# Optimization experiments

Measured on AMD Instinct MI355X. Metric: run time of the kernel, lower is better.

The kernel has to match this reference:

```python
import jax, jax.numpy as jnp
import numpy as np

B = 65536          # batch
E = 512            # embedding_dim
SL = 128           # speed_latent_dim
H = 256            # hidden_size
NB = 6             # num_branch
D = E + SL         # 640, branch input dim


def _linear_init(k, din, dout):
    bound = 1.0 / np.sqrt(din)
    kw, kb = jax.random.split(k)
    W = jax.random.uniform(kw, (din, dout), minval=-bound, maxval=bound, dtype=jnp.float32)
    b = jax.random.uniform(kb, (dout,), minval=-bound, maxval=bound, dtype=jnp.float32)
    return W, b


def setup_inputs() -> dict:
    key = jax.random.key(0)
    ks = jax.random.split(key, 10)
    embedding = jax.random.normal(ks[0], (B, E), dtype=jnp.float32)
    speed = jax.random.uniform(ks[1], (B, 1), dtype=jnp.float32)
    command = jax.random.randint(ks[2], (B,), 1, NB + 1)  # values in 1..6

    # speed_in: Linear(1,H) -> ReLU -> Linear(H,SL)
    si_W1, si_b1 = _linear_init(ks[3], 1, H)
    si_W2, si_b2 = _linear_init(ks[4], H, SL)

    # speed_out: Linear(D,H) -> ReLU -> Linear(H,H) -> ReLU -> Linear(H,1)
    so_W1, so_b1 = _linear_init(ks[5], D, H)
    so_W2, so_b2 = _linear_init(ks[6], H, H)
    so_W3, so_b3 = _linear_init(ks[7], H, 1)

    # NB branches, each Linear(D,H)->ReLU->Linear(H,H)->ReLU->Linear(H,3)->Sigmoid
    def mk_branch(k):
        k1, k2, k3 = jax.random.split(k, 3)
        W1, b1 = _linear_init(k1, D, H)
        W2, b2 = _linear_init(k2, H, H)
        W3, b3 = _linear_init(k3, H, 3)
        return W1, b1, W2, b2, W3, b3

    bW1, bb1, bW2, bb2, bW3, bb3 = jax.vmap(mk_branch)(jax.random.split(ks[8], NB))

    return {
        "embedding": embedding, "speed": speed, "command": command,
        "si_W1": si_W1, "si_b1": si_b1, "si_W2": si_W2, "si_b2": si_b2,
        "bW1": bW1, "bb1": bb1, "bW2": bW2, "bb2": bb2, "bW3": bW3, "bb3": bb3,
        "so_W1": so_W1, "so_b1": so_b1, "so_W2": so_W2, "so_b2": so_b2,
        "so_W3": so_W3, "so_b3": so_b3,
    }


def reference(embedding, speed, command,
              si_W1, si_b1, si_W2, si_b2,
              bW1, bb1, bW2, bb2, bW3, bb3,
              so_W1, so_b1, so_W2, so_b2, so_W3, so_b3):
    # speed_in MLP and concat
    s = jax.nn.relu(speed @ si_W1 + si_b1) @ si_W2 + si_b2          # [B, SL]
    emb = jnp.concatenate([embedding, s], axis=1)                    # [B, D]

    # all branches computed densely (as in the torch module), then one-hot mask
    h1 = jax.nn.relu(jnp.einsum('bd,ndh->nbh', emb, bW1) + bb1[:, None, :])   # [NB,B,H]
    h2 = jax.nn.relu(jnp.einsum('nbh,nhk->nbk', h1, bW2) + bb2[:, None, :])   # [NB,B,H]
    out = jax.nn.sigmoid(jnp.einsum('nbk,nko->nbo', h2, bW3) + bb3[:, None, :])  # [NB,B,3]

    mask = (jnp.arange(NB)[:, None] == (command - 1)[None, :]).astype(out.dtype)  # [NB,B]
    control_pred = jnp.sum(out * mask[:, :, None], axis=0)           # [B, 3]

    # speed prediction head
    sp = jax.nn.relu(emb @ so_W1 + so_b1)
    sp = jax.nn.relu(sp @ so_W2 + so_b2)
    speed_pred = sp @ so_W3 + so_b3                                  # [B, 1]

    return control_pred, speed_pred
```

## Files before the change

### kernel.cpp

```cpp
#include <hip/hip_runtime.h>
#include <cstdint>
#include <cstddef>

typedef _Float16 f16;
typedef f16 f16x8 __attribute__((ext_vector_type(8)));
typedef float f32x4 __attribute__((ext_vector_type(4)));

#define B_ROWS 65536
#define NT_BRANCH 1030
#define NT_SPEED 1024

constexpr size_t OFF_SF16   = 0;
constexpr size_t SZ_SF16    = (size_t)B_ROWS * 128 * 2;
constexpr size_t OFF_SIW2T  = OFF_SF16 + SZ_SF16;
constexpr size_t SZ_SIW2T   = (size_t)128 * 256 * 2;
constexpr size_t OFF_BW1T   = OFF_SIW2T + SZ_SIW2T;
constexpr size_t SZ_BW1T    = (size_t)6 * 256 * 640 * 2;
constexpr size_t OFF_BW2T   = OFF_BW1T + SZ_BW1T;
constexpr size_t SZ_BW2T    = (size_t)6 * 256 * 256 * 2;
constexpr size_t OFF_SOW1T  = OFF_BW2T + SZ_BW2T;
constexpr size_t SZ_SOW1T   = (size_t)256 * 640 * 2;
constexpr size_t OFF_SOW2T  = OFF_SOW1T + SZ_SOW1T;
constexpr size_t SZ_SOW2T   = (size_t)256 * 256 * 2;
constexpr size_t OFF_BW3T16 = OFF_SOW2T + SZ_SOW2T;
constexpr size_t SZ_BW3T16  = (size_t)6 * 16 * 256 * 2;
constexpr size_t OFF_SOW3T16= OFF_BW3T16 + SZ_BW3T16;
constexpr size_t SZ_SOW3T16 = (size_t)16 * 256 * 2;
constexpr size_t OFF_COUNTS = OFF_SOW3T16 + SZ_SOW3T16;
constexpr size_t OFF_CURSORS= OFF_COUNTS + 256;
constexpr size_t OFF_BINBASE= OFF_CURSORS + 256;
constexpr size_t OFF_TILECMD= OFF_BINBASE + 256;
constexpr size_t OFF_PERM   = OFF_TILECMD + 4352;
constexpr size_t WS_NEEDED  = OFF_PERM + (size_t)NT_BRANCH * 64 * 4;

#define MFMA16(a, b, c) __builtin_amdgcn_mfma_f32_16x16x32_f16(a, b, c, 0, 0, 0)
#define BARSYNC() asm volatile("s_waitcnt lgkmcnt(0)\n\ts_barrier" ::: "memory")

__global__ void prep_kernel(const float* __restrict__ siW2,
                            const float* __restrict__ bW1,
                            const float* __restrict__ bW2,
                            const float* __restrict__ soW1,
                            const float* __restrict__ soW2,
                            const float* __restrict__ bW3,
                            const float* __restrict__ soW3,
                            f16* __restrict__ siW2T, f16* __restrict__ bW1T,
                            f16* __restrict__ bW2T, f16* __restrict__ soW1T,
                            f16* __restrict__ soW2T,
                            f16* __restrict__ bW3T16, f16* __restrict__ soW3T16,
                            int* __restrict__ counts, int* __restrict__ cursors,
                            int* __restrict__ perm)
{
    const int bx = blockIdx.x;
    const int tx = threadIdx.x, ty = threadIdx.y;
    const int tid = ty * 32 + tx;
    if (bx >= 1601) {
        const int ib = bx - 1601;
        const int idx = ib * 256 + tid;
        if (idx < NT_BRANCH * 64) perm[idx] = -1;
        if (ib == 0 && tid < 6) { counts[tid] = 0; cursors[tid] = 0; }
        return;
    }
    if (bx == 1600) {
        for (int i = tid; i < 6 * 16 * 256; i += 256) {
            const int c = i >> 12, rem = i & 4095, n = rem >> 8, k = rem & 255;
            bW3T16[i] = (n < 3) ? (f16)bW3[((size_t)c * 256 + k) * 3 + n] : (f16)0;
        }
        for (int i = tid; i < 16 * 256; i += 256) {
            const int n = i >> 8, k = i & 255;
            soW3T16[i] = (n == 0) ? (f16)soW3[k] : (f16)0;
        }
        return;
    }
    const float* in; f16* out; int R, C, lb;
    if (bx < 960)       { int m = bx / 160;        lb = bx - m * 160;       in = bW1 + (size_t)m * 640 * 256; out = bW1T + (size_t)m * 640 * 256; R = 640; C = 256; }
    else if (bx < 1344) { int m = (bx - 960) / 64; lb = (bx - 960) - m * 64; in = bW2 + (size_t)m * 256 * 256; out = bW2T + (size_t)m * 256 * 256; R = 256; C = 256; }
    else if (bx < 1504) { lb = bx - 1344; in = soW1; out = soW1T; R = 640; C = 256; }
    else if (bx < 1568) { lb = bx - 1504; in = soW2; out = soW2T; R = 256; C = 256; }
    else                { lb = bx - 1568; in = siW2; out = siW2T; R = 256; C = 128; }
    const int txt = C >> 5;
    const int c0 = (lb % txt) << 5;
    const int r0 = (lb / txt) << 5;
    __shared__ float tile[32][33];
    #pragma unroll
    for (int i = 0; i < 4; ++i)
        tile[tx][ty + 8 * i] = in[(size_t)(r0 + ty + 8 * i) * C + c0 + tx];
    __syncthreads();
    #pragma unroll
    for (int i = 0; i < 4; ++i)
        out[(size_t)(c0 + ty + 8 * i) * R + r0 + tx] = (f16)tile[ty + 8 * i][tx];
}

__global__ __launch_bounds__(256) void speedin_kernel(
    const float* __restrict__ speed,
    const float* __restrict__ siW1, const float* __restrict__ sib1,
    const f16* __restrict__ siW2T, const float* __restrict__ sib2,
    const int* __restrict__ cmd,
    f16* __restrict__ sF16, int* __restrict__ counts)
{
    __shared__ f16 H[64 * 264];
    __shared__ float spd[64];
    __shared__ int h[6];
    const int tid = threadIdx.x;
    const int rb = blockIdx.x * 64;
    if (tid < 6) h[tid] = 0;
    __syncthreads();
    if (tid < 64) {
        spd[tid] = speed[rb + tid];
        atomicAdd(&h[cmd[rb + tid] - 1], 1);
    }
    __syncthreads();
    if (tid < 6 && h[tid] > 0) atomicAdd(&counts[tid], h[tid]);
    {
        const float w1 = siW1[tid], b1v = sib1[tid];
        #pragma unroll 4
        for (int r = 0; r < 64; ++r) {
            float hv = spd[r] * w1 + b1v;
            H[r * 264 + tid] = (f16)(hv > 0.f ? hv : 0.f);
        }
    }
    __syncthreads();
    const int w = tid >> 6, lane = tid & 63, lq = lane >> 4, l16 = lane & 15;
    const int nb = w * 32;
    f32x4 acc[4][2];
    #pragma unroll
    for (int mt = 0; mt < 4; ++mt)
        #pragma unroll
        for (int nt = 0; nt < 2; ++nt)
            acc[mt][nt] = (f32x4){0.f, 0.f, 0.f, 0.f};
    for (int ks = 0; ks < 8; ++ks) {
        const int koff = ks * 32 + lq * 8;
        f16x8 af[4], bf[2];
        #pragma unroll
        for (int mt = 0; mt < 4; ++mt)
            af[mt] = *(const f16x8*)(&H[(mt * 16 + l16) * 264 + koff]);
        #pragma unroll
        for (int nt = 0; nt < 2; ++nt)
            bf[nt] = *(const f16x8*)(siW2T + (size_t)(nb + nt * 16 + l16) * 256 + koff);
        #pragma unroll
        for (int mt = 0; mt < 4; ++mt)
            #pragma unroll
            for (int nt = 0; nt < 2; ++nt)
                acc[mt][nt] = MFMA16(af[mt], bf[nt], acc[mt][nt]);
    }
    #pragma unroll
    for (int mt = 0; mt < 4; ++mt)
        #pragma unroll
        for (int nt = 0; nt < 2; ++nt) {
            const int n = nb + nt * 16 + l16;
            const float bv = sib2[n];
            #pragma unroll
            for (int r2 = 0; r2 < 4; ++r2) {
                const int m = mt * 16 + lq * 4 + r2;
                sF16[(size_t)(rb + m) * 128 + n] = (f16)(acc[mt][nt][r2] + bv);
            }
        }
}

__global__ void plan_kernel(const int* __restrict__ counts,
                            int* __restrict__ binBase, int* __restrict__ tile_cmd) {
    __shared__ int tbase[7];
    if (threadIdx.x == 0) {
        int base = 0, tb = 0;
        for (int c = 0; c < 6; ++c) {
            binBase[c] = base;
            tbase[c] = tb;
            const int nt = (counts[c] + 63) >> 6;
            tb += nt;
            base += nt << 6;
        }
        tbase[6] = tb;
    }
    __syncthreads();
    for (int t = threadIdx.x; t < NT_BRANCH; t += 256) {
        int c = -1;
        #pragma unroll
        for (int j = 0; j < 6; ++j)
            if (t >= tbase[j] && t < tbase[j + 1]) c = j;
        tile_cmd[t] = c;
    }
}

__global__ void place_kernel(const int* __restrict__ cmd,
                             const int* __restrict__ binBase,
                             int* __restrict__ cursors, int* __restrict__ perm) {
    __shared__ int lcnt[6], lbase[6];
    const int tid = threadIdx.x;
    if (tid < 6) lcnt[tid] = 0;
    __syncthreads();
    const int i = blockIdx.x * 256 + tid;
    const int c = cmd[i] - 1;
    const int myr = atomicAdd(&lcnt[c], 1);
    __syncthreads();
    if (tid < 6) lbase[tid] = atomicAdd(&cursors[tid], lcnt[tid]);
    __syncthreads();
    perm[binBase[c] + lbase[c] + myr] = i;
}

__device__ __forceinline__ f16x8 stage_load(const float* __restrict__ srcF,
                                            const f16* __restrict__ srcH,
                                            int kc, int p) {
    if (kc < 8) {
        const float* s = srcF + kc * 64 + p * 8;
        const float4 f0 = ((const float4*)s)[0];
        const float4 f1 = ((const float4*)s)[1];
        f16x8 v;
        v[0] = (f16)f0.x; v[1] = (f16)f0.y; v[2] = (f16)f0.z; v[3] = (f16)f0.w;
        v[4] = (f16)f1.x; v[5] = (f16)f1.y; v[6] = (f16)f1.z; v[7] = (f16)f1.w;
        return v;
    } else {
        return *(const f16x8*)(srcH + (kc - 8) * 64 + p * 8);
    }
}

__global__ __launch_bounds__(512, 4) void heads_kernel(
    const float* __restrict__ emb,
    const f16* __restrict__ sF16,
    const int* __restrict__ perm, const int* __restrict__ tile_cmd,
    const f16* __restrict__ bW1T, const f16* __restrict__ bW2T,
    const f16* __restrict__ bW3T16,
    const float* __restrict__ bb1, const float* __restrict__ bb2,
    const float* __restrict__ bb3,
    const f16* __restrict__ soW1T, const f16* __restrict__ soW2T,
    const f16* __restrict__ soW3T16,
    const float* __restrict__ sob1, const float* __restrict__ sob2,
    const float* __restrict__ sob3,
    float* __restrict__ out)
{
    __shared__ f16 smem[16896];
    __shared__ int rowIdx[64];
    const int bx = blockIdx.x;
    const int tid = threadIdx.x;
    const bool is_speed = (bx >= NT_BRANCH);
    const f16 *W1T, *W2T, *W3T;
    const float *bias1, *bias2, *bias3;
    if (is_speed) {
        const int t = bx - NT_BRANCH;
        if (tid < 64) rowIdx[tid] = t * 64 + tid;
        W1T = soW1T; W2T = soW2T; W3T = soW3T16;
        bias1 = sob1; bias2 = sob2; bias3 = sob3;
    } else {
        const int c = tile_cmd[bx];
        if (c < 0) return;
        if (tid < 64) rowIdx[tid] = perm[bx * 64 + tid];
        W1T = bW1T + (size_t)c * 256 * 640;
        W2T = bW2T + (size_t)c * 256 * 256;
        W3T = bW3T16 + (size_t)c * 16 * 256;
        bias1 = bb1 + c * 256; bias2 = bb2 + c * 256; bias3 = bb3 + c * 3;
    }
    __syncthreads();

    const int r = tid >> 3, p = tid & 7;
    int growS = rowIdx[r]; if (growS < 0) growS = 0;
    const float* srcF = emb + (size_t)growS * 512;
    const f16*   srcH = sF16 + (size_t)growS * 128;
    const int pOff = r * 72 + p * 8;

    const int w = tid >> 6, lane = tid & 63, lq = lane >> 4, l16 = lane & 15;
    const int nb = w * 32;
    const f16* brow[2];
    #pragma unroll
    for (int nt = 0; nt < 2; ++nt)
        brow[nt] = W1T + (size_t)(nb + nt * 16 + l16) * 640;

    f32x4 acc[4][2];
    #pragma unroll
    for (int mt = 0; mt < 4; ++mt)
        #pragma unroll
        for (int nt = 0; nt < 2; ++nt)
            acc[mt][nt] = (f32x4){0.f, 0.f, 0.f, 0.f};

    f16x8 sreg[4];
    f16x8 Bb[2][2][2];
    #pragma unroll
    for (int j = 0; j < 4; ++j)
        sreg[j] = stage_load(srcF, srcH, j, p);
    #pragma unroll
    for (int ks = 0; ks < 2; ++ks)
        #pragma unroll
        for (int nt = 0; nt < 2; ++nt) {
            Bb[0][ks][nt] = *(const f16x8*)(brow[nt] + 0 * 64 + ks * 32 + lq * 8);
            Bb[1][ks][nt] = *(const f16x8*)(brow[nt] + 1 * 64 + ks * 32 + lq * 8);
        }
    *(f16x8*)(smem + pOff) = sreg[0];
    BARSYNC();
    #pragma unroll
    for (int kc = 0; kc < 10; ++kc) {
        f16* cur = smem + (kc & 1) * 4608;
        if (kc < 9)
            *(f16x8*)(smem + ((kc + 1) & 1) * 4608 + pOff) = sreg[(kc + 1) & 3];
        if (kc < 6)
            sreg[kc & 3] = stage_load(srcF, srcH, kc + 4, p);
        #pragma unroll
        for (int ks = 0; ks < 2; ++ks) {
            f16x8 a[4];
            #pragma unroll
            for (int mt = 0; mt < 4; ++mt)
                a[mt] = *(const f16x8*)(cur + (mt * 16 + l16) * 72 + ks * 32 + lq * 8);
            #pragma unroll
            for (int mt = 0; mt < 4; ++mt)
                #pragma unroll
                for (int nt = 0; nt < 2; ++nt)
                    acc[mt][nt] = MFMA16(a[mt], Bb[kc & 1][ks][nt], acc[mt][nt]);
        }
        if (kc < 8) {
            #pragma unroll
            for (int ks = 0; ks < 2; ++ks)
                #pragma unroll
                for (int nt = 0; nt < 2; ++nt)
                    Bb[kc & 1][ks][nt] = *(const f16x8*)(brow[nt] + (kc + 2) * 64 + ks * 32 + lq * 8);
        }
        BARSYNC();
    }

    const f16* brow2[2];
    #pragma unroll
    for (int nt = 0; nt < 2; ++nt)
        brow2[nt] = W2T + (size_t)(nb + nt * 16 + l16) * 256;
    f16x8 Bd[2][2];
    #pragma unroll
    for (int nt = 0; nt < 2; ++nt)
        Bd[0][nt] = *(const f16x8*)(brow2[nt] + lq * 8);

    #pragma unroll
    for (int mt = 0; mt < 4; ++mt)
        #pragma unroll
        for (int nt = 0; nt < 2; ++nt) {
            const int n = nb + nt * 16 + l16;
            const float bv = bias1[n];
            #pragma unroll
            for (int r2 = 0; r2 < 4; ++r2) {
                const int m = mt * 16 + lq * 4 + r2;
                const float v = acc[mt][nt][r2] + bv;
                smem[m * 264 + n] = (f16)(v > 0.f ? v : 0.f);
            }
            acc[mt][nt] = (f32x4){0.f, 0.f, 0.f, 0.f};
        }
    BARSYNC();

    #pragma unroll
    for (int ks = 0; ks < 8; ++ks) {
        if (ks < 7) {
            #pragma unroll
            for (int nt = 0; nt < 2; ++nt)
                Bd[(ks + 1) & 1][nt] = *(const f16x8*)(brow2[nt] + (ks + 1) * 32 + lq * 8);
        }
        f16x8 a[4];
        #pragma unroll
        for (int mt = 0; mt < 4; ++mt)
            a[mt] = *(const f16x8*)(&smem[(mt * 16 + l16) * 264 + ks * 32 + lq * 8]);
        #pragma unroll
        for (int mt = 0; mt < 4; ++mt)
            #pragma unroll
            for (int nt = 0; nt < 2; ++nt)
                acc[mt][nt] = MFMA16(a[mt], Bd[ks & 1][nt], acc[mt][nt]);
    }
    BARSYNC();
    #pragma unroll
    for (int mt = 0; mt < 4; ++mt)
        #pragma unroll
        for (int nt = 0; nt < 2; ++nt) {
            const int n = nb + nt * 16 + l16;
            const float bv = bias2[n];
            #pragma unroll
            for (int r2 = 0; r2 < 4; ++r2) {
                const int m = mt * 16 + lq * 4 + r2;
                const float v = acc[mt][nt][r2] + bv;
                smem[m * 264 + n] = (f16)(v > 0.f ? v : 0.f);
            }
        }
    BARSYNC();
    if (w < 4) {
        f32x4 acc3 = (f32x4){0.f, 0.f, 0.f, 0.f};
        const f16* w3row = W3T + (size_t)l16 * 256;
        #pragma unroll
        for (int ks = 0; ks < 8; ++ks) {
            const int koff = ks * 32 + lq * 8;
            const f16x8 af = *(const f16x8*)(&smem[(w * 16 + l16) * 264 + koff]);
            const f16x8 bf = *(const f16x8*)(w3row + koff);
            acc3 = MFMA16(af, bf, acc3);
        }
        const int orow = w * 16 + lq * 4;
        if (!is_speed) {
            if (l16 < 3) {
                const float b3 = bias3[l16];
                #pragma unroll
                for (int r2 = 0; r2 < 4; ++r2) {
                    const int g = rowIdx[orow + r2];
                    if (g >= 0)
                        out[(size_t)g * 3 + l16] = 1.f / (1.f + __expf(-(acc3[r2] + b3)));
                }
            }
        } else {
            if (l16 == 0) {
                const float b3 = bias3[0];
                #pragma unroll
                for (int r2 = 0; r2 < 4; ++r2)
                    out[(size_t)3 * B_ROWS + rowIdx[orow + r2]] = acc3[r2] + b3;
            }
        }
    }
}

extern "C" void kernel_launch(void* const* d_in, const int* in_sizes, int n_in,
                              void* d_out, int out_size, void* d_ws, size_t ws_size,
                              hipStream_t stream) {
    (void)in_sizes; (void)n_in; (void)out_size; (void)ws_size;
    const float* embedding = (const float*)d_in[0];
    const float* speed     = (const float*)d_in[1];
    const int*   command   = (const int*)d_in[2];
    const float* si_W1 = (const float*)d_in[3];
    const float* si_b1 = (const float*)d_in[4];
    const float* si_W2 = (const float*)d_in[5];
    const float* si_b2 = (const float*)d_in[6];
    const float* bW1   = (const float*)d_in[7];
    const float* bb1   = (const float*)d_in[8];
    const float* bW2   = (const float*)d_in[9];
    const float* bb2   = (const float*)d_in[10];
    const float* bW3   = (const float*)d_in[11];
    const float* bb3   = (const float*)d_in[12];
    const float* so_W1 = (const float*)d_in[13];
    const float* so_b1 = (const float*)d_in[14];
    const float* so_W2 = (const float*)d_in[15];
    const float* so_b2 = (const float*)d_in[16];
    const float* so_W3 = (const float*)d_in[17];
    const float* so_b3 = (const float*)d_in[18];
    float* out = (float*)d_out;

    char* ws = (char*)d_ws;
    f16* sF16   = (f16*)(ws + OFF_SF16);
    f16* siW2T  = (f16*)(ws + OFF_SIW2T);
    f16* bW1T   = (f16*)(ws + OFF_BW1T);
    f16* bW2T   = (f16*)(ws + OFF_BW2T);
    f16* soW1T  = (f16*)(ws + OFF_SOW1T);
    f16* soW2T  = (f16*)(ws + OFF_SOW2T);
    f16* bW3T16 = (f16*)(ws + OFF_BW3T16);
    f16* soW3T16= (f16*)(ws + OFF_SOW3T16);
    int* counts = (int*)(ws + OFF_COUNTS);
    int* cursors= (int*)(ws + OFF_CURSORS);
    int* binBase= (int*)(ws + OFF_BINBASE);
    int* tile_cmd = (int*)(ws + OFF_TILECMD);
    int* perm   = (int*)(ws + OFF_PERM);

    prep_kernel<<<1859, dim3(32, 8), 0, stream>>>(
        si_W2, bW1, bW2, so_W1, so_W2, bW3, so_W3,
        siW2T, bW1T, bW2T, soW1T, soW2T, bW3T16, soW3T16,
        counts, cursors, perm);
    speedin_kernel<<<1024, 256, 0, stream>>>(
        speed, si_W1, si_b1, siW2T, si_b2, command, sF16, counts);
    plan_kernel<<<1, 256, 0, stream>>>(counts, binBase, tile_cmd);
    place_kernel<<<256, 256, 0, stream>>>(command, binBase, cursors, perm);
    heads_kernel<<<NT_BRANCH + NT_SPEED, 512, 0, stream>>>(
        embedding, sF16, perm, tile_cmd,
        bW1T, bW2T, bW3T16, bb1, bb2, bb3,
        soW1T, soW2T, soW3T16, so_b1, so_b2, so_b3, out);
}
```

Before: 380.9 us.

## Stage layer-1 activations in two half-K LDS chunks instead of double-buffered 64-col tiles

Replaces the per-64-column double-buffered LDS pipeline for the first GEMM with two large staging phases. Each phase loads 320 columns of the activation row, converts them to fp16 and stores them in a 64x328 LDS tile. The second half is prefetched into registers while the first half is being consumed. This cuts the block-wide barriers from about ten to a handful and issues the global loads in larger batches. In exchange it uses more LDS and more registers per thread (float4 staging arrays), which may lower occupancy under launch_bounds(512,4).

```diff
diff --git a/kernel.cpp b/kernel.cpp
--- a/kernel.cpp
+++ b/kernel.cpp
@@ -196,19 +196,40 @@
     perm[binBase[c] + lbase[c] + myr] = i;
 }
 
-__device__ __forceinline__ f16x8 stage_load(const float* __restrict__ srcF,
-                                            const f16* __restrict__ srcH,
-                                            int kc, int p) {
-    if (kc < 8) {
-        const float* s = srcF + kc * 64 + p * 8;
-        const float4 f0 = ((const float4*)s)[0];
-        const float4 f1 = ((const float4*)s)[1];
-        f16x8 v;
-        v[0] = (f16)f0.x; v[1] = (f16)f0.y; v[2] = (f16)f0.z; v[3] = (f16)f0.w;
-        v[4] = (f16)f1.x; v[5] = (f16)f1.y; v[6] = (f16)f1.z; v[7] = (f16)f1.w;
-        return v;
-    } else {
-        return *(const f16x8*)(srcH + (kc - 8) * 64 + p * 8);
+template<bool PREF>
+__device__ __forceinline__ void kc_iter(const f16* __restrict__ smem,
+                                        const f16* __restrict__ brow0,
+                                        const f16* __restrict__ brow1,
+                                        f16x8 (&Bb)[2][2], f32x4 (&acc)[4][2],
+                                        int LCOL, int NGCOL, int l16, int lq)
+{
+    f16x8 Bn[2][2];
+    if (PREF) {
+        #pragma unroll
+        for (int ks = 0; ks < 2; ++ks) {
+            Bn[ks][0] = *(const f16x8*)(brow0 + NGCOL + ks * 32 + lq * 8);
+            Bn[ks][1] = *(const f16x8*)(brow1 + NGCOL + ks * 32 + lq * 8);
+        }
+    }
+    f16x8 a_[2][4];
+    #pragma unroll
+    for (int ks = 0; ks < 2; ++ks)
+        #pragma unroll
+        for (int mt = 0; mt < 4; ++mt)
+            a_[ks][mt] = *(const f16x8*)(smem + (mt * 16 + l16) * 328 + LCOL + ks * 32 + lq * 8);
+    #pragma unroll
+    for (int ks = 0; ks < 2; ++ks)
+        #pragma unroll
+        for (int mt = 0; mt < 4; ++mt)
+            #pragma unroll
+            for (int nt = 0; nt < 2; ++nt)
+                acc[mt][nt] = MFMA16(a_[ks][mt], Bb[ks][nt], acc[mt][nt]);
+    if (PREF) {
+        #pragma unroll
+        for (int ks = 0; ks < 2; ++ks)
+            #pragma unroll
+            for (int nt = 0; nt < 2; ++nt)
+                Bb[ks][nt] = Bn[ks][nt];
     }
 }
 
@@ -226,7 +247,7 @@
     const float* __restrict__ sob3,
     float* __restrict__ out)
 {
-    __shared__ f16 smem[16896];
+    __shared__ f16 smem[64 * 328];
     __shared__ int rowIdx[64];
     const int bx = blockIdx.x;
     const int tid = threadIdx.x;
@@ -253,14 +274,36 @@
     int growS = rowIdx[r]; if (growS < 0) growS = 0;
     const float* srcF = emb + (size_t)growS * 512;
     const f16*   srcH = sF16 + (size_t)growS * 128;
-    const int pOff = r * 72 + p * 8;
+    const int wOff = r * 328 + p * 8;
 
     const int w = tid >> 6, lane = tid & 63, lq = lane >> 4, l16 = lane & 15;
     const int nb = w * 32;
-    const f16* brow[2];
-    #pragma unroll
-    for (int nt = 0; nt < 2; ++nt)
-        brow[nt] = W1T + (size_t)(nb + nt * 16 + l16) * 640;
+    const f16* brow0 = W1T + (size_t)(nb + l16) * 640;
+    const f16* brow1 = W1T + (size_t)(nb + 16 + l16) * 640;
+
+    f16x8 Bb[2][2];
+    #pragma unroll
+    for (int ks = 0; ks < 2; ++ks) {
+        Bb[ks][0] = *(const f16x8*)(brow0 + ks * 32 + lq * 8);
+        Bb[ks][1] = *(const f16x8*)(brow1 + ks * 32 + lq * 8);
+    }
+
+    float4 s0[5][2];
+    #pragma unroll
+    for (int c = 0; c < 5; ++c) {
+        const float* s = srcF + c * 64 + p * 8;
+        s0[c][0] = ((const float4*)s)[0];
+        s0[c][1] = ((const float4*)s)[1];
+    }
+    #pragma unroll
+    for (int c = 0; c < 5; ++c) {
+        f16x8 v;
+        v[0] = (f16)s0[c][0].x; v[1] = (f16)s0[c][0].y;
+        v[2] = (f16)s0[c][0].z; v[3] = (f16)s0[c][0].w;
+        v[4] = (f16)s0[c][1].x; v[5] = (f16)s0[c][1].y;
+        v[6] = (f16)s0[c][1].z; v[7] = (f16)s0[c][1].w;
+        *(f16x8*)(smem + wOff + c * 64) = v;
+    }
 
     f32x4 acc[4][2];
     #pragma unroll
@@ -269,48 +312,45 @@
         for (int nt = 0; nt < 2; ++nt)
             acc[mt][nt] = (f32x4){0.f, 0.f, 0.f, 0.f};
 
-    f16x8 sreg[4];
-    f16x8 Bb[2][2][2];
-    #pragma unroll
-    for (int j = 0; j < 4; ++j)
-        sreg[j] = stage_load(srcF, srcH, j, p);
-    #pragma unroll
-    for (int ks = 0; ks < 2; ++ks)
-        #pragma unroll
-        for (int nt = 0; nt < 2; ++nt) {
-            Bb[0][ks][nt] = *(const f16x8*)(brow[nt] + 0 * 64 + ks * 32 + lq * 8);
-            Bb[1][ks][nt] = *(const f16x8*)(brow[nt] + 1 * 64 + ks * 32 + lq * 8);
-        }
-    *(f16x8*)(smem + pOff) = sreg[0];
-    BARSYNC();
-    #pragma unroll
-    for (int kc = 0; kc < 10; ++kc) {
-        f16* cur = smem + (kc & 1) * 4608;
-        if (kc < 9)
-            *(f16x8*)(smem + ((kc + 1) & 1) * 4608 + pOff) = sreg[(kc + 1) & 3];
-        if (kc < 6)
-            sreg[kc & 3] = stage_load(srcF, srcH, kc + 4, p);
-        #pragma unroll
-        for (int ks = 0; ks < 2; ++ks) {
-            f16x8 a[4];
-            #pragma unroll
-            for (int mt = 0; mt < 4; ++mt)
-                a[mt] = *(const f16x8*)(cur + (mt * 16 + l16) * 72 + ks * 32 + lq * 8);
-            #pragma unroll
-            for (int mt = 0; mt < 4; ++mt)
-                #pragma unroll
-                for (int nt = 0; nt < 2; ++nt)
-                    acc[mt][nt] = MFMA16(a[mt], Bb[kc & 1][ks][nt], acc[mt][nt]);
-        }
-        if (kc < 8) {
-            #pragma unroll
-            for (int ks = 0; ks < 2; ++ks)
-                #pragma unroll
-                for (int nt = 0; nt < 2; ++nt)
-                    Bb[kc & 1][ks][nt] = *(const f16x8*)(brow[nt] + (kc + 2) * 64 + ks * 32 + lq * 8);
-        }
-        BARSYNC();
-    }
+    BARSYNC();
+
+    kc_iter<true>(smem, brow0, brow1, Bb, acc,   0,  64, l16, lq);
+    kc_iter<true>(smem, brow0, brow1, Bb, acc,  64, 128, l16, lq);
+    kc_iter<true>(smem, brow0, brow1, Bb, acc, 128, 192, l16, lq);
+
+    float4 s1[3][2];
+    f16x8 t1[2];
+    #pragma unroll
+    for (int c = 0; c < 3; ++c) {
+        const float* s = srcF + 320 + c * 64 + p * 8;
+        s1[c][0] = ((const float4*)s)[0];
+        s1[c][1] = ((const float4*)s)[1];
+    }
+    t1[0] = *(const f16x8*)(srcH + p * 8);
+    t1[1] = *(const f16x8*)(srcH + 64 + p * 8);
+
+    kc_iter<true>(smem, brow0, brow1, Bb, acc, 192, 256, l16, lq);
+    kc_iter<true>(smem, brow0, brow1, Bb, acc, 256, 320, l16, lq);
+
+    BARSYNC();
+    #pragma unroll
+    for (int c = 0; c < 3; ++c) {
+        f16x8 v;
+        v[0] = (f16)s1[c][0].x; v[1] = (f16)s1[c][0].y;
+        v[2] = (f16)s1[c][0].z; v[3] = (f16)s1[c][0].w;
+        v[4] = (f16)s1[c][1].x; v[5] = (f16)s1[c][1].y;
+        v[6] = (f16)s1[c][1].z; v[7] = (f16)s1[c][1].w;
+        *(f16x8*)(smem + wOff + c * 64) = v;
+    }
+    *(f16x8*)(smem + wOff + 192) = t1[0];
+    *(f16x8*)(smem + wOff + 256) = t1[1];
+    BARSYNC();
+
+    kc_iter<true >(smem, brow0, brow1, Bb, acc,   0, 384, l16, lq);
+    kc_iter<true >(smem, brow0, brow1, Bb, acc,  64, 448, l16, lq);
+    kc_iter<true >(smem, brow0, brow1, Bb, acc, 128, 512, l16, lq);
+    kc_iter<true >(smem, brow0, brow1, Bb, acc, 192, 576, l16, lq);
+    kc_iter<false>(smem, brow0, brow1, Bb, acc, 256,   0, l16, lq);
 
     const f16* brow2[2];
     #pragma unroll
@@ -320,6 +360,8 @@
     #pragma unroll
     for (int nt = 0; nt < 2; ++nt)
         Bd[0][nt] = *(const f16x8*)(brow2[nt] + lq * 8);
+
+    BARSYNC();
 
     #pragma unroll
     for (int mt = 0; mt < 4; ++mt)
```

After: 399.8 us. 1.05x slower.

## Double row tile to 128 per block to halve weight reloads

Applied to the files above, without the earlier changes.

Each heads_kernel block now processes 128 rows instead of 64. Each wave keeps 8x2 accumulator tiles, and the shared staging buffer and register staging are widened to match. The aim is to halve per-row weight traffic from global memory and amortize the block setup and barriers over more rows. In exchange, register and LDS pressure rise, occupancy drops (launch bounds go from 4 to 3), there are half as many blocks for load balance, and partially filled bins pad more rows.

```diff
diff --git a/kernel.cpp b/kernel.cpp
--- a/kernel.cpp
+++ b/kernel.cpp
@@ -7,8 +7,9 @@
 typedef float f32x4 __attribute__((ext_vector_type(4)));
 
 #define B_ROWS 65536
-#define NT_BRANCH 1030
-#define NT_SPEED 1024
+#define TILE_M 128
+#define NT_BRANCH 518
+#define NT_SPEED 512
 
 constexpr size_t OFF_SF16   = 0;
 constexpr size_t SZ_SF16    = (size_t)B_ROWS * 128 * 2;
@@ -31,7 +32,7 @@
 constexpr size_t OFF_BINBASE= OFF_CURSORS + 256;
 constexpr size_t OFF_TILECMD= OFF_BINBASE + 256;
 constexpr size_t OFF_PERM   = OFF_TILECMD + 4352;
-constexpr size_t WS_NEEDED  = OFF_PERM + (size_t)NT_BRANCH * 64 * 4;
+constexpr size_t WS_NEEDED  = OFF_PERM + (size_t)NT_BRANCH * TILE_M * 4;
 
 #define MFMA16(a, b, c) __builtin_amdgcn_mfma_f32_16x16x32_f16(a, b, c, 0, 0, 0)
 #define BARSYNC() asm volatile("s_waitcnt lgkmcnt(0)\n\ts_barrier" ::: "memory")
@@ -56,7 +57,7 @@
     if (bx >= 1601) {
         const int ib = bx - 1601;
         const int idx = ib * 256 + tid;
-        if (idx < NT_BRANCH * 64) perm[idx] = -1;
+        if (idx < NT_BRANCH * TILE_M) perm[idx] = -1;
         if (ib == 0 && tid < 6) { counts[tid] = 0; cursors[tid] = 0; }
         return;
     }
@@ -164,9 +165,9 @@
         for (int c = 0; c < 6; ++c) {
             binBase[c] = base;
             tbase[c] = tb;
-            const int nt = (counts[c] + 63) >> 6;
+            const int nt = (counts[c] + TILE_M - 1) >> 7;
             tb += nt;
-            base += nt << 6;
+            base += nt << 7;
         }
         tbase[6] = tb;
     }
@@ -196,23 +197,29 @@
     perm[binBase[c] + lbase[c] + myr] = i;
 }
 
-__device__ __forceinline__ f16x8 stage_load(const float* __restrict__ srcF,
+__device__ __forceinline__ void stage_load2(const float* __restrict__ srcF,
                                             const f16* __restrict__ srcH,
-                                            int kc, int p) {
+                                            int kc, int p, f16x8* v) {
     if (kc < 8) {
-        const float* s = srcF + kc * 64 + p * 8;
+        const float* s = srcF + kc * 64 + p * 16;
         const float4 f0 = ((const float4*)s)[0];
         const float4 f1 = ((const float4*)s)[1];
-        f16x8 v;
-        v[0] = (f16)f0.x; v[1] = (f16)f0.y; v[2] = (f16)f0.z; v[3] = (f16)f0.w;
-        v[4] = (f16)f1.x; v[5] = (f16)f1.y; v[6] = (f16)f1.z; v[7] = (f16)f1.w;
-        return v;
+        const float4 f2 = ((const float4*)s)[2];
+        const float4 f3 = ((const float4*)s)[3];
+        f16x8 a, b;
+        a[0] = (f16)f0.x; a[1] = (f16)f0.y; a[2] = (f16)f0.z; a[3] = (f16)f0.w;
+        a[4] = (f16)f1.x; a[5] = (f16)f1.y; a[6] = (f16)f1.z; a[7] = (f16)f1.w;
+        b[0] = (f16)f2.x; b[1] = (f16)f2.y; b[2] = (f16)f2.z; b[3] = (f16)f2.w;
+        b[4] = (f16)f3.x; b[5] = (f16)f3.y; b[6] = (f16)f3.z; b[7] = (f16)f3.w;
+        v[0] = a; v[1] = b;
     } else {
-        return *(const f16x8*)(srcH + (kc - 8) * 64 + p * 8);
-    }
-}
-
-__global__ __launch_bounds__(512, 4) void heads_kernel(
+        const f16* s = srcH + (kc - 8) * 64 + p * 16;
+        v[0] = ((const f16x8*)s)[0];
+        v[1] = ((const f16x8*)s)[1];
+    }
+}
+
+__global__ __launch_bounds__(512, 3) void heads_kernel(
     const float* __restrict__ emb,
     const f16* __restrict__ sF16,
     const int* __restrict__ perm, const int* __restrict__ tile_cmd,
@@ -226,8 +233,8 @@
     const float* __restrict__ sob3,
     float* __restrict__ out)
 {
-    __shared__ f16 smem[16896];
-    __shared__ int rowIdx[64];
+    __shared__ f16 smem[33792];
+    __shared__ int rowIdx[TILE_M];
     const int bx = blockIdx.x;
     const int tid = threadIdx.x;
     const bool is_speed = (bx >= NT_BRANCH);
@@ -235,13 +242,13 @@
     const float *bias1, *bias2, *bias3;
     if (is_speed) {
         const int t = bx - NT_BRANCH;
-        if (tid < 64) rowIdx[tid] = t * 64 + tid;
+        if (tid < TILE_M) rowIdx[tid] = t * TILE_M + tid;
         W1T = soW1T; W2T = soW2T; W3T = soW3T16;
         bias1 = sob1; bias2 = sob2; bias3 = sob3;
     } else {
         const int c = tile_cmd[bx];
         if (c < 0) return;
-        if (tid < 64) rowIdx[tid] = perm[bx * 64 + tid];
+        if (tid < TILE_M) rowIdx[tid] = perm[bx * TILE_M + tid];
         W1T = bW1T + (size_t)c * 256 * 640;
         W2T = bW2T + (size_t)c * 256 * 256;
         W3T = bW3T16 + (size_t)c * 16 * 256;
@@ -249,65 +256,76 @@
     }
     __syncthreads();
 
-    const int r = tid >> 3, p = tid & 7;
+    const int r = tid >> 2, p = tid & 3;
     int growS = rowIdx[r]; if (growS < 0) growS = 0;
     const float* srcF = emb + (size_t)growS * 512;
     const f16*   srcH = sF16 + (size_t)growS * 128;
-    const int pOff = r * 72 + p * 8;
+    const int pOff = r * 72 + p * 16;
 
     const int w = tid >> 6, lane = tid & 63, lq = lane >> 4, l16 = lane & 15;
     const int nb = w * 32;
-    const f16* brow[2];
-    #pragma unroll
-    for (int nt = 0; nt < 2; ++nt)
-        brow[nt] = W1T + (size_t)(nb + nt * 16 + l16) * 640;
-
-    f32x4 acc[4][2];
-    #pragma unroll
-    for (int mt = 0; mt < 4; ++mt)
+    const f16* brow0 = W1T + (size_t)(nb + l16) * 640;
+    const f16* brow1 = W1T + (size_t)(nb + 16 + l16) * 640;
+
+    f32x4 acc[8][2];
+    #pragma unroll
+    for (int mt = 0; mt < 8; ++mt)
         #pragma unroll
         for (int nt = 0; nt < 2; ++nt)
             acc[mt][nt] = (f32x4){0.f, 0.f, 0.f, 0.f};
 
-    f16x8 sreg[4];
-    f16x8 Bb[2][2][2];
-    #pragma unroll
-    for (int j = 0; j < 4; ++j)
-        sreg[j] = stage_load(srcF, srcH, j, p);
-    #pragma unroll
-    for (int ks = 0; ks < 2; ++ks)
-        #pragma unroll
-        for (int nt = 0; nt < 2; ++nt) {
-            Bb[0][ks][nt] = *(const f16x8*)(brow[nt] + 0 * 64 + ks * 32 + lq * 8);
-            Bb[1][ks][nt] = *(const f16x8*)(brow[nt] + 1 * 64 + ks * 32 + lq * 8);
-        }
-    *(f16x8*)(smem + pOff) = sreg[0];
+    f16x8 sreg[3][2];
+    #pragma unroll
+    for (int j = 0; j < 3; ++j)
+        stage_load2(srcF, srcH, j, p, sreg[j]);
+    f16x8 Bb[2][2];
+    #pragma unroll
+    for (int ks = 0; ks < 2; ++ks) {
+        Bb[ks][0] = *(const f16x8*)(brow0 + ks * 32 + lq * 8);
+        Bb[ks][1] = *(const f16x8*)(brow1 + ks * 32 + lq * 8);
+    }
+    *(f16x8*)(smem + pOff) = sreg[0][0];
+    *(f16x8*)(smem + pOff + 8) = sreg[0][1];
     BARSYNC();
+
     #pragma unroll
     for (int kc = 0; kc < 10; ++kc) {
-        f16* cur = smem + (kc & 1) * 4608;
-        if (kc < 9)
-            *(f16x8*)(smem + ((kc + 1) & 1) * 4608 + pOff) = sreg[(kc + 1) & 3];
-        if (kc < 6)
-            sreg[kc & 3] = stage_load(srcF, srcH, kc + 4, p);
-        #pragma unroll
-        for (int ks = 0; ks < 2; ++ks) {
-            f16x8 a[4];
-            #pragma unroll
-            for (int mt = 0; mt < 4; ++mt)
-                a[mt] = *(const f16x8*)(cur + (mt * 16 + l16) * 72 + ks * 32 + lq * 8);
-            #pragma unroll
-            for (int mt = 0; mt < 4; ++mt)
+        const f16* cur = smem + (kc & 1) * 9216;
+        if (kc < 9) {
+            f16* dst = smem + ((kc + 1) & 1) * 9216 + pOff;
+            *(f16x8*)(dst)     = sreg[(kc + 1) % 3][0];
+            *(f16x8*)(dst + 8) = sreg[(kc + 1) % 3][1];
+        }
+        if (kc < 7)
+            stage_load2(srcF, srcH, kc + 3, p, sreg[kc % 3]);
+        f16x8 Bn[2][2];
+        if (kc < 9) {
+            #pragma unroll
+            for (int ks = 0; ks < 2; ++ks) {
+                Bn[ks][0] = *(const f16x8*)(brow0 + (kc + 1) * 64 + ks * 32 + lq * 8);
+                Bn[ks][1] = *(const f16x8*)(brow1 + (kc + 1) * 64 + ks * 32 + lq * 8);
+            }
+        }
+        #pragma unroll
+        for (int ks = 0; ks < 2; ++ks)
+            #pragma unroll
+            for (int mh = 0; mh < 2; ++mh) {
+                f16x8 a[4];
                 #pragma unroll
-                for (int nt = 0; nt < 2; ++nt)
-                    acc[mt][nt] = MFMA16(a[mt], Bb[kc & 1][ks][nt], acc[mt][nt]);
-        }
-        if (kc < 8) {
+                for (int mt = 0; mt < 4; ++mt)
+                    a[mt] = *(const f16x8*)(cur + ((mh * 4 + mt) * 16 + l16) * 72 + ks * 32 + lq * 8);
+                #pragma unroll
+                for (int mt = 0; mt < 4; ++mt) {
+                    acc[mh * 4 + mt][0] = MFMA16(a[mt], Bb[ks][0], acc[mh * 4 + mt][0]);
+                    acc[mh * 4 + mt][1] = MFMA16(a[mt], Bb[ks][1], acc[mh * 4 + mt][1]);
+                }
+            }
+        if (kc < 9) {
             #pragma unroll
             for (int ks = 0; ks < 2; ++ks)
                 #pragma unroll
                 for (int nt = 0; nt < 2; ++nt)
-                    Bb[kc & 1][ks][nt] = *(const f16x8*)(brow[nt] + (kc + 2) * 64 + ks * 32 + lq * 8);
+                    Bb[ks][nt] = Bn[ks][nt];
         }
         BARSYNC();
     }
@@ -322,7 +340,7 @@
         Bd[0][nt] = *(const f16x8*)(brow2[nt] + lq * 8);
 
     #pragma unroll
-    for (int mt = 0; mt < 4; ++mt)
+    for (int mt = 0; mt < 8; ++mt)
         #pragma unroll
         for (int nt = 0; nt < 2; ++nt) {
             const int n = nb + nt * 16 + l16;
@@ -344,19 +362,22 @@
             for (int nt = 0; nt < 2; ++nt)
                 Bd[(ks + 1) & 1][nt] = *(const f16x8*)(brow2[nt] + (ks + 1) * 32 + lq * 8);
         }
-        f16x8 a[4];
-        #pragma unroll
-        for (int mt = 0; mt < 4; ++mt)
-            a[mt] = *(const f16x8*)(&smem[(mt * 16 + l16) * 264 + ks * 32 + lq * 8]);
-        #pragma unroll
-        for (int mt = 0; mt < 4; ++mt)
-            #pragma unroll
-            for (int nt = 0; nt < 2; ++nt)
-                acc[mt][nt] = MFMA16(a[mt], Bd[ks & 1][nt], acc[mt][nt]);
+        #pragma unroll
+        for (int mh = 0; mh < 2; ++mh) {
+            f16x8 a[4];
+            #pragma unroll
+            for (int mt = 0; mt < 4; ++mt)
+                a[mt] = *(const f16x8*)(&smem[((mh * 4 + mt) * 16 + l16) * 264 + ks * 32 + lq * 8]);
+            #pragma unroll
+            for (int mt = 0; mt < 4; ++mt) {
+                acc[mh * 4 + mt][0] = MFMA16(a[mt], Bd[ks & 1][0], acc[mh * 4 + mt][0]);
+                acc[mh * 4 + mt][1] = MFMA16(a[mt], Bd[ks & 1][1], acc[mh * 4 + mt][1]);
+            }
+        }
     }
     BARSYNC();
     #pragma unroll
-    for (int mt = 0; mt < 4; ++mt)
+    for (int mt = 0; mt < 8; ++mt)
         #pragma unroll
         for (int nt = 0; nt < 2; ++nt) {
             const int n = nb + nt * 16 + l16;
@@ -369,7 +390,7 @@
             }
         }
     BARSYNC();
-    if (w < 4) {
+    {
         f32x4 acc3 = (f32x4){0.f, 0.f, 0.f, 0.f};
         const f16* w3row = W3T + (size_t)l16 * 256;
         #pragma unroll
@@ -394,8 +415,11 @@
             if (l16 == 0) {
                 const float b3 = bias3[0];
                 #pragma unroll
-                for (int r2 = 0; r2 < 4; ++r2)
-                    out[(size_t)3 * B_ROWS + rowIdx[orow + r2]] = acc3[r2] + b3;
+                for (int r2 = 0; r2 < 4; ++r2) {
+                    const int g = rowIdx[orow + r2];
+                    if (g >= 0)
+                        out[(size_t)3 * B_ROWS + g] = acc3[r2] + b3;
+                }
             }
         }
     }
@@ -441,7 +465,7 @@
     int* tile_cmd = (int*)(ws + OFF_TILECMD);
     int* perm   = (int*)(ws + OFF_PERM);
 
-    prep_kernel<<<1859, dim3(32, 8), 0, stream>>>(
+    prep_kernel<<<1860, dim3(32, 8), 0, stream>>>(
         si_W2, bW1, bW2, so_W1, so_W2, bW3, so_W3,
         siW2T, bW1T, bW2T, soW1T, soW2T, bW3T16, soW3T16,
         counts, cursors, perm);
```

New measurement: 366.0 us. 1.04x faster.
